# Performance work log

Measured on AMD Instinct MI355X. Metric: run time of the kernel, lower is better.

The kernel has to match this reference:

```python
import math
import jax, jax.numpy as jnp
import numpy as np
from jax import lax

B, H, L, DK = 2, 8, 512, 16
DM = H * DK            # conv channels = d_k * h
NK = int(math.floor(math.log2(L))) + 1   # 10 scales, kernel sizes 2^g+1
KMAX = 2 ** (NK - 1)   # 512: max causal padding
KS = KMAX + 1          # 513: padded (shared) kernel length


def setup_inputs() -> dict:
    key = jax.random.key(0)
    ks = jax.random.split(key, NK + 6)
    Q = jax.random.normal(ks[0], (B, H, L, DK), jnp.float32)
    K = jax.random.normal(ks[1], (B, H, L, DK), jnp.float32)
    V = jax.random.normal(ks[2], (B, H, L, DK), jnp.float32)
    # Per-scale Conv1d weights, left-zero-padded to a shared kernel length KS.
    # Scale g has true kernel size 2^g+1 occupying the trailing taps.
    W = jnp.zeros((NK, DM, DM, KS), jnp.float32)
    for g in range(NK):
        klen = 2 ** g + 1
        W = W.at[g, :, :, KS - klen:].set(
            jax.random.normal(ks[3 + g], (DM, DM, klen), jnp.float32) * 0.02)
    b_conv = jax.random.normal(ks[3 + NK], (NK, DM), jnp.float32) * 0.02
    causal = jnp.triu(jnp.ones((L, L), bool), 1)          # True = masked
    attn_mask = jnp.broadcast_to(causal, (B, H, L, L))
    return dict(Q=Q, K=K, V=V, W=W, b_conv=b_conv, attn_mask=attn_mask)


def _multiscale(x_flat, W, b_conv):
    # x_flat: [B, L, DM] (raw reshape of [B,H,L,DK], matching torch .reshape)
    # Left-pad by KMAX once; each zero-padded kernel then reproduces the
    # per-scale causal conv (pad=2^g, kernel=2^g+1) exactly.
    xp = jnp.pad(jnp.transpose(x_flat, (0, 2, 1)), ((0, 0), (0, 0), (KMAX, 0)))  # [B,DM,L+KMAX]

    def conv1(w, bb):  # w: [DM, DM, KS], bb: [DM]
        y = lax.conv_general_dilated(xp, w, (1,), 'VALID',
                                     dimension_numbers=('NCH', 'OIH', 'NCH'))
        return y + bb[None, :, None]                       # [B, DM, L]

    y = jax.vmap(conv1)(W, b_conv)                         # [NK, B, DM, L]
    # torch: conv_out.reshape(b, h, l, d_k) -- raw row-major reinterpretation
    y = y.reshape(NK, B, H, L, DK)
    return jnp.transpose(y, (1, 2, 0, 3, 4))               # [B, H, NK, L, DK]


def reference(Q, K, V, W, b_conv, attn_mask):
    # 'con' branch: V is discarded and replaced by the multi-scale K.
    Qf = Q.reshape(B, L, DM)          # raw reshape, as in the torch code
    Kf = K.reshape(B, L, DM)
    Q_p = _multiscale(Qf, W, b_conv)  # [B,H,NK,L,DK]
    K_p = _multiscale(Kf, W, b_conv)  # [B,H,NK,L,DK]
    scores = jnp.einsum('bhgqd,bhgkd->bhgqk', Q_p, K_p) / math.sqrt(DK)
    scores = jnp.where(attn_mask[:, :, None, :, :], jnp.float32(-1e9), scores)
    attn = jax.nn.softmax(scores, axis=2)                  # softmax over scales (dim=-3)
    context = jnp.einsum('bhgqk,bhgkd->bhqd', attn, K_p)   # V := K_p
    attn_out = attn.sum(axis=2)                            # einsum('bhgqk->bhqk')
    return context, attn_out
```

## Files before the change

kernel.cpp:

```cpp
#include <hip/hip_runtime.h>

#define Bv 2
#define Hv 8
#define Lv 512
#define DKv 16
#define DMv 128
#define NKv 10
#define KSv 513

typedef __attribute__((ext_vector_type(8))) short short8;
typedef __attribute__((ext_vector_type(4))) float f32x4;

__device__ __constant__ int d_nc[10]     = {1,1,1,1,2,3,5,9,17,33};
__device__ __constant__ int d_cumnc[10]  = {0,1,2,3,4,6,9,14,23,40};

#define Y_BYTES   (10485760)
#define XR_OFF    (Y_BYTES)
#define WB_OFF    (Y_BYTES + 524288)

__device__ inline unsigned short f2bf(float f) {
    unsigned u = __float_as_uint(f);
    unsigned r = (u + 0x7FFFu + ((u >> 16) & 1u)) >> 16;
    return (unsigned short)r;
}

__global__ __launch_bounds__(256) void prep_repack(const float* __restrict__ Q,
                                                   const float* __restrict__ K,
                                                   const float* __restrict__ W,
                                                   unsigned short* __restrict__ xr,
                                                   unsigned short* __restrict__ wb,
                                                   float4* __restrict__ Y4,
                                                   float4* __restrict__ out4) {
    __shared__ float tile[128][17];
    int bid0 = blockIdx.x;
    int tid = threadIdx.x;

    if (bid0 < 9344) {
        int cid = bid0 >> 7;
        int o = bid0 & 127;
        int g, rem = cid;
#pragma unroll
        for (g = 0; g < 10; ++g) { int nc = d_nc[g]; if (rem < nc) break; rem -= nc; }
        int cl = rem;
        int w_g = d_nc[g] * 16;
        int ccol = w_g - 16 * (cl + 1);
        int wcolbase = 513 - w_g + ccol;

        const float* wsrc = W + (size_t)g * 16384 * 513 + (size_t)o * 128 * 513;
        int rr = tid >> 4, cc = tid & 15;
        int col = wcolbase + cc;
        for (int r = rr; r < 128; r += 16) {
            float v = 0.f;
            if (col >= 0) v = wsrc[(size_t)r * 513 + col];
            tile[r][cc] = v;
        }
        __syncthreads();

        unsigned short* wdst = wb + (size_t)262144 * d_cumnc[g];
        int c2 = tid >> 4;
        int s  = tid & 15;
        int ib = s >> 2, qv = s & 3;
        int i0 = ib * 32 + qv * 8;
        unsigned short pack[8];
#pragma unroll
        for (int e = 0; e < 8; ++e) pack[e] = f2bf(tile[i0 + e][c2]);
        size_t off = (size_t)(ccol + c2) * 16384 +
                     (((o >> 4) * 4 + ib) * 512 + (o & 15) * 32 + qv * 8);
        *(short8*)(wdst + off) = *(short8*)pack;
    } else {
        int stride = 2048 * 256;
        for (int i = (bid0 - 9344) * 256 + tid; i < 1507328; i += stride) {
            if (i < 196608) {
                Y4[131072 + i] = make_float4(0.f, 0.f, 0.f, 0.f);
            } else if (i < 393216) {
                Y4[458752 + (i - 196608)] = make_float4(0.f, 0.f, 0.f, 0.f);
            } else if (i < 1441792) {
                out4[32768 + (i - 393216)] = make_float4(1.f, 1.f, 1.f, 1.f);
            } else {
                int idx = i - 1441792;
                int flat = idx * 4;
                int p = flat >> 17;
                int off = flat & 131071;
                const float* src = p ? K : Q;
                float4 v = *(const float4*)(src + off);
                ushort4 o4;
                o4.x = f2bf(v.x); o4.y = f2bf(v.y); o4.z = f2bf(v.z); o4.w = f2bf(v.w);
                *(ushort4*)(xr + flat) = o4;
            }
        }
    }
}

__global__ __launch_bounds__(256, 2) void conv_mfma(const unsigned short* __restrict__ xr,
                                                    const unsigned short* __restrict__ wb,
                                                    float* __restrict__ Y) {
    int j = blockIdx.x;
    int r = j & 7, yy = (j >> 3) & 7, qq = j >> 6;
    int cid = qq * 8 + r;
    if (cid >= 73) return;
    int g, rem = cid;
#pragma unroll
    for (g = 0; g < 10; ++g) { int nc = d_nc[g]; if (rem < nc) break; rem -= nc; }
    int cl = rem;
    int w_g = d_nc[g] * 16;
    int ccol = w_g - 16 * (cl + 1);

    int p = yy >> 2, b = (yy >> 1) & 1, tt = yy & 1;
    int t0 = tt * 256;
    int pb = yy >> 1;

    int xbase = t0 + 1 - 16 * (cl + 1);
    if (xbase < -270) return;

    __shared__ unsigned short xs[272 * 128];

    int tid = threadIdx.x;
    const unsigned short* xp = xr + (size_t)pb * 65536;
    for (int e = tid; e < 272 * 16; e += 256) {
        int u = e >> 4, ic = e & 15;
        int xi = xbase + u;
        short8 v = (short8)0;
        if (xi >= 0 && xi < 512) v = *(const short8*)(xp + (size_t)xi * 128 + ic * 8);
        *(short8*)(&xs[u * 128 + (((ic + u) & 15) << 3)]) = v;
    }
    __syncthreads();

    int lane = tid & 63, wv = tid >> 6;
    int wm = wv >> 1, wn = wv & 1;
    int l15 = lane & 15, q = lane >> 4;

    const unsigned short* wgp = wb + (size_t)262144 * d_cumnc[g] + (size_t)ccol * 16384;
    int abase = l15 * 32 + q * 8;

    f32x4 acc[4][8];
#pragma unroll
    for (int mt = 0; mt < 4; ++mt)
#pragma unroll
        for (int nt = 0; nt < 8; ++nt) acc[mt][nt] = (f32x4)0.f;

    short8 a0[4], a1[4], b0[8], b1[8];

#define LOADAB(A, B, KK) { \
    int jjx = (KK) >> 2, ibx = (KK) & 3; \
    const unsigned short* tpx = wgp + (size_t)jjx * 16384; \
    int row0x = wn * 128 + l15 + jjx; \
    _Pragma("unroll") for (int mt = 0; mt < 4; ++mt) \
        A[mt] = *(const short8*)(tpx + ((wm * 4 + mt) * 4 + ibx) * 512 + abase); \
    _Pragma("unroll") for (int nt = 0; nt < 8; ++nt) { \
        int rowx = row0x + nt * 16; \
        B[nt] = *(const short8*)(&xs[rowx * 128 + (((ibx * 4 + q + rowx) & 15) << 3)]); \
    } }

#define FMAAB(A, B) { \
    _Pragma("unroll") for (int mt = 0; mt < 4; ++mt) \
    _Pragma("unroll") for (int nt = 0; nt < 8; ++nt) \
        acc[mt][nt] = __builtin_amdgcn_mfma_f32_16x16x32_bf16(A[mt], B[nt], acc[mt][nt], 0, 0, 0); }

    LOADAB(a0, b0, 0);
    for (int kk = 0; kk < 64; kk += 2) {
        LOADAB(a1, b1, kk + 1);
        FMAAB(a0, b0);
        if (kk + 2 < 64) LOADAB(a0, b0, kk + 2);
        FMAAB(a1, b1);
    }
#undef LOADAB
#undef FMAAB

    float* yp = Y + (((size_t)p * NKv + g) * 2 + b) * 65536;
    int orow = wm * 64 + q * 4;
    int tcol = t0 + wn * 128 + l15;
    if (cid <= 3) {
#pragma unroll
        for (int mt = 0; mt < 4; ++mt)
#pragma unroll
            for (int nt = 0; nt < 8; ++nt)
#pragma unroll
                for (int rr = 0; rr < 4; ++rr)
                    yp[(size_t)(orow + mt * 16 + rr) * 512 + tcol + nt * 16] =
                        acc[mt][nt][rr];
    } else {
#pragma unroll
        for (int mt = 0; mt < 4; ++mt)
#pragma unroll
            for (int nt = 0; nt < 8; ++nt)
#pragma unroll
                for (int rr = 0; rr < 4; ++rr)
                    atomicAdd(&yp[(size_t)(orow + mt * 16 + rr) * 512 + tcol + nt * 16],
                              acc[mt][nt][rr]);
    }
}

__global__ __launch_bounds__(512) void suffix_ctx(const float* __restrict__ Y,
                                                  const float* __restrict__ bconv,
                                                  float* __restrict__ out) {
    int blk = blockIdx.x;
    int bh = blk >> 4, d = blk & 15;
    int b = bh >> 3, h = bh & 7;
    int k = threadIdx.x;
    int o = h * 16 + (k >> 5);
    int t = (k & 31) * 16 + d;

    float S = 0.f;
#pragma unroll
    for (int g = 0; g < NKv; ++g)
        S += Y[(((size_t)(NKv + g) * 2 + b) * 65536) + (size_t)o * 512 + t]
           + bconv[g * 128 + o];

    __shared__ float sc[512];
    sc[k] = S;
    __syncthreads();
    float v = S;
    for (int ofs = 1; ofs < 512; ofs <<= 1) {
        float add = (k + ofs < 512) ? sc[k + ofs] : 0.f;
        __syncthreads();
        v += add;
        sc[k] = v;
        __syncthreads();
    }
    out[(((size_t)b * 8 + h) * 512 + k) * 16 + d] = 0.1f * (v - S);
}

__global__ __launch_bounds__(512) void attn_phase2(const float* __restrict__ Y,
                                                   const float* __restrict__ bconv,
                                                   float* __restrict__ out) {
    int blk = blockIdx.x;
    int half = blk & 1;
    int pr = blk >> 1;
    int bh = pr >> 3;
    int qp = pr & 7;
    int b = bh >> 3, h = bh & 7;

    int qtA = qp, qtB = 15 - qp;
    int u0 = half ? 8 : 0, u1 = half ? 17 : 8;

    __shared__ float Qs[2][NKv * 640];
    __shared__ float Ks[NKv * 640];

    int tid = threadIdx.x;

#pragma unroll
    for (int X = 0; X < 2; ++X) {
        int o = h * 16 + (X ? qtB : qtA);
        for (int e = tid; e < NKv * 128; e += 512) {
            int g = e >> 7, c = e & 127;
            float4 v = *(const float4*)(Y + (((size_t)g * 2 + b) * 65536) +
                                        (size_t)o * 512 + c * 4);
            float bb = bconv[g * 128 + o];
            int qq2 = c >> 2, dd = c & 3;
            *(float4*)&Qs[X][g * 640 + qq2 * 20 + dd * 4] =
                make_float4(v.x + bb, v.y + bb, v.z + bb, v.w + bb);
        }
    }

    int q = (tid >> 4) & 31;
    int kl = tid & 15;
    float ctx[16];
#pragma unroll
    for (int d = 0; d < 16; ++d) ctx[d] = 0.f;
    int curX = (u0 <= qtA) ? 0 : 1;

    for (int u = u0; u < u1; ++u) {
        int X = (u <= qtA) ? 0 : 1;
        int qt = X ? qtB : qtA;
        int kt = X ? (u - qtA - 1) : u;

        if (X != curX) {
            int pqt = curX ? qtB : qtA;
#pragma unroll
            for (int d = 0; d < 16; ++d) {
                float v = ctx[d];
                v += __shfl_xor(v, 1);
                v += __shfl_xor(v, 2);
                v += __shfl_xor(v, 4);
                v += __shfl_xor(v, 8);
                if (kl == 0)
                    atomicAdd(&out[(((size_t)b * 8 + h) * 512 + pqt * 32 + q) * 16 + d], v);
                ctx[d] = 0.f;
            }
            curX = X;
        }

        __syncthreads();
        int o_k = h * 16 + kt;
        for (int e = tid; e < NKv * 128; e += 512) {
            int g = e >> 7, c = e & 127;
            float4 v = *(const float4*)(Y + (((size_t)(NKv + g) * 2 + b) * 65536) +
                                        (size_t)o_k * 512 + c * 4);
            float bb = bconv[g * 128 + o_k];
            int kk = c >> 2, dd = c & 3;
            *(float4*)&Ks[g * 640 + kk * 20 + dd * 4] =
                make_float4(v.x + bb, v.y + bb, v.z + bb, v.w + bb);
        }
        __syncthreads();

        int qg = qt * 32 + q;
        bool dg = (kt == qt);

        float m[2] = {-1e30f, -1e30f};
        float l[2] = {0.f, 0.f};
        float ca[2][16];
#pragma unroll
        for (int ki = 0; ki < 2; ++ki)
#pragma unroll
            for (int d = 0; d < 16; ++d) ca[ki][d] = 0.f;

        for (int g = 0; g < NKv; ++g) {
            const float* Qg = &Qs[X][g * 640 + q * 20];
            float4 qv0 = *(const float4*)(Qg);
            float4 qv1 = *(const float4*)(Qg + 4);
            float4 qv2 = *(const float4*)(Qg + 8);
            float4 qv3 = *(const float4*)(Qg + 12);
#pragma unroll
            for (int ki = 0; ki < 2; ++ki) {
                const float* Kg = &Ks[g * 640 + (ki * 16 + kl) * 20];
                float kv[16];
                *(float4*)&kv[0]  = *(const float4*)(Kg);
                *(float4*)&kv[4]  = *(const float4*)(Kg + 4);
                *(float4*)&kv[8]  = *(const float4*)(Kg + 8);
                *(float4*)&kv[12] = *(const float4*)(Kg + 12);
                float s = 0.f;
                s = fmaf(qv0.x, kv[0], s);  s = fmaf(qv0.y, kv[1], s);
                s = fmaf(qv0.z, kv[2], s);  s = fmaf(qv0.w, kv[3], s);
                s = fmaf(qv1.x, kv[4], s);  s = fmaf(qv1.y, kv[5], s);
                s = fmaf(qv1.z, kv[6], s);  s = fmaf(qv1.w, kv[7], s);
                s = fmaf(qv2.x, kv[8], s);  s = fmaf(qv2.y, kv[9], s);
                s = fmaf(qv2.z, kv[10], s); s = fmaf(qv2.w, kv[11], s);
                s = fmaf(qv3.x, kv[12], s); s = fmaf(qv3.y, kv[13], s);
                s = fmaf(qv3.z, kv[14], s); s = fmaf(qv3.w, kv[15], s);
                s *= 0.25f;
                float mn = fmaxf(m[ki], s);
                float sc = __expf(m[ki] - mn);
                float w  = __expf(s - mn);
                m[ki] = mn;
                l[ki] = l[ki] * sc + w;
#pragma unroll
                for (int d = 0; d < 16; ++d)
                    ca[ki][d] = fmaf(ca[ki][d], sc, w * kv[d]);
            }
        }

#pragma unroll
        for (int ki = 0; ki < 2; ++ki) {
            int kg = kt * 32 + ki * 16 + kl;
            float inv = (dg && kg > qg) ? 0.f : (1.f / l[ki]);
#pragma unroll
            for (int d = 0; d < 16; ++d) ctx[d] = fmaf(ca[ki][d], inv, ctx[d]);
        }
    }

    int pqt = curX ? qtB : qtA;
#pragma unroll
    for (int d = 0; d < 16; ++d) {
        float v = ctx[d];
        v += __shfl_xor(v, 1);
        v += __shfl_xor(v, 2);
        v += __shfl_xor(v, 4);
        v += __shfl_xor(v, 8);
        if (kl == 0)
            atomicAdd(&out[(((size_t)b * 8 + h) * 512 + pqt * 32 + q) * 16 + d], v);
    }
}

extern "C" void kernel_launch(void* const* d_in, const int* in_sizes, int n_in,
                              void* d_out, int out_size, void* d_ws, size_t ws_size,
                              hipStream_t stream) {
    const float* Q = (const float*)d_in[0];
    const float* K = (const float*)d_in[1];
    const float* W = (const float*)d_in[3];
    const float* bconv = (const float*)d_in[4];
    float* out = (float*)d_out;

    float* Y = (float*)d_ws;
    unsigned short* xr = (unsigned short*)((char*)d_ws + XR_OFF);
    unsigned short* wb = (unsigned short*)((char*)d_ws + WB_OFF);

    prep_repack<<<11392, 256, 0, stream>>>(Q, K, W, xr, wb, (float4*)Y, (float4*)out);

    conv_mfma<<<640, 256, 0, stream>>>(xr, wb, Y);

    suffix_ctx<<<256, 512, 0, stream>>>(Y, bconv, out);

    attn_phase2<<<256, 512, 0, stream>>>(Y, bconv, out);
}
```

Baseline: 199.3 us.

## Replace atomic accumulation of large-scale conv chunks with scratch partials plus reduction

For the scale chunks with cid >= 9, conv blocks now write their partial results with plain stores into a scratch buffer instead of using float atomicAdd into Y. A new reduce_part kernel sums the partials per scale and writes them into Y. This is meant to remove contention and the cost of atomic traffic, at the price of an extra kernel launch and about 64 MB of extra scratch writes and reads. The path is taken only when the workspace is large enough.

New measurement: 186.7 us. -6.3%, faster.

```diff
diff --git a/kernel.cpp b/kernel.cpp
--- a/kernel.cpp
+++ b/kernel.cpp
@@ -17,6 +17,8 @@
 #define Y_BYTES   (10485760)
 #define XR_OFF    (Y_BYTES)
 #define WB_OFF    (Y_BYTES + 524288)
+#define PART_OFF  (WB_OFF + 38273024)
+#define PART_BYTES (67108864)
 
 __device__ inline unsigned short f2bf(float f) {
     unsigned u = __float_as_uint(f);
@@ -93,7 +95,9 @@
 
 __global__ __launch_bounds__(256, 2) void conv_mfma(const unsigned short* __restrict__ xr,
                                                     const unsigned short* __restrict__ wb,
-                                                    float* __restrict__ Y) {
+                                                    float* __restrict__ Y,
+                                                    float* __restrict__ part,
+                                                    int use_scratch) {
     int j = blockIdx.x;
     int r = j & 7, yy = (j >> 3) & 7, qq = j >> 6;
     int cid = qq * 8 + r;
@@ -166,8 +170,22 @@
 #undef LOADAB
 #undef FMAAB
 
+    int orow = wm * 64 + q * 4;
+    if (cid >= 9 && use_scratch) {
+        float* pp = part + ((size_t)(cid - 9) * 8 + yy) * 32768;
+        int tloc = wn * 128 + l15;
+#pragma unroll
+        for (int mt = 0; mt < 4; ++mt)
+#pragma unroll
+            for (int nt = 0; nt < 8; ++nt)
+#pragma unroll
+                for (int rr = 0; rr < 4; ++rr)
+                    pp[(size_t)(orow + mt * 16 + rr) * 256 + tloc + nt * 16] =
+                        acc[mt][nt][rr];
+        return;
+    }
+
     float* yp = Y + (((size_t)p * NKv + g) * 2 + b) * 65536;
-    int orow = wm * 64 + q * 4;
     int tcol = t0 + wn * 128 + l15;
     if (cid <= 3) {
 #pragma unroll
@@ -188,6 +206,36 @@
                     atomicAdd(&yp[(size_t)(orow + mt * 16 + rr) * 512 + tcol + nt * 16],
                               acc[mt][nt][rr]);
     }
+}
+
+__global__ __launch_bounds__(256) void reduce_part(const float4* __restrict__ part4,
+                                                   float4* __restrict__ Y4) {
+    int idx = blockIdx.x * 256 + threadIdx.x;
+    if (idx >= 262144) return;
+    int gg  = idx >> 16;
+    int rem = idx & 65535;
+    int pbi = rem >> 14;
+    int r2  = rem & 16383;
+    int o   = r2 >> 7;
+    int tc4 = r2 & 127;
+    int tt  = tc4 >> 6;
+    int tl4 = tc4 & 63;
+
+    const int cb[4]  = {0, 5, 14, 31};
+    const int nch[4] = {5, 9, 17, 33};
+    int n = nch[gg];
+    int clmax = tt ? 32 : 16;
+    if (n > clmax) n = clmax;
+    int base = cb[gg];
+    int yy = pbi * 2 + tt;
+
+    float4 s = make_float4(0.f, 0.f, 0.f, 0.f);
+    for (int cl = 0; cl < n; ++cl) {
+        float4 v = part4[((size_t)(base + cl) * 8 + yy) * 8192 + o * 64 + tl4];
+        s.x += v.x; s.y += v.y; s.z += v.z; s.w += v.w;
+    }
+    int p = pbi >> 1, b = pbi & 1;
+    Y4[(((size_t)p * NKv + 6 + gg) * 2 + b) * 16384 + o * 128 + tc4] = s;
 }
 
 __global__ __launch_bounds__(512) void suffix_ctx(const float* __restrict__ Y,
@@ -373,10 +421,15 @@
     float* Y = (float*)d_ws;
     unsigned short* xr = (unsigned short*)((char*)d_ws + XR_OFF);
     unsigned short* wb = (unsigned short*)((char*)d_ws + WB_OFF);
+    float* part = (float*)((char*)d_ws + PART_OFF);
+    int use_scratch = (ws_size >= (size_t)PART_OFF + PART_BYTES) ? 1 : 0;
 
     prep_repack<<<11392, 256, 0, stream>>>(Q, K, W, xr, wb, (float4*)Y, (float4*)out);
 
-    conv_mfma<<<640, 256, 0, stream>>>(xr, wb, Y);
+    conv_mfma<<<640, 256, 0, stream>>>(xr, wb, Y, part, use_scratch);
+
+    if (use_scratch)
+        reduce_part<<<1024, 256, 0, stream>>>((const float4*)part, (float4*)Y);
 
     suffix_ctx<<<256, 512, 0, stream>>>(Y, bconv, out);
 
```
